# Performance work log

Measured on AMD Instinct MI355X. Metric: run time of the kernel, lower is better.

Reference implementation:

```python
import jax, jax.numpy as jnp
import numpy as np
import math

IMG_SIZE = 768
NUM_CLASSES = 90
THRESHOLD = 0.05
IOU_THRESHOLD = 0.5
MAX_DETECTIONS = 100
K_CAND = 512  # per-class candidate pool before greedy NMS
RATIOS = [(1.0, 1.0), (1.4, 0.7), (0.7, 1.4)]
SCALES = [2 ** 0, 2 ** (1.0 / 3.0), 2 ** (2.0 / 3.0)]


def _generate_anchors():
    anchor_scale = 4.0
    pyramid_levels = [3, 4, 5, 6, 7]
    all_levels = []
    for lv in pyramid_levels:
        stride = 2 ** lv
        size = anchor_scale * 2 ** lv
        grid = IMG_SIZE // stride
        sx = np.arange(grid) * stride
        sy, sx = np.meshgrid(np.arange(grid) * stride, sx, indexing='ij')
        # torch meshgrid(shift_y, shift_x, indexing='ij') -> rows are y
        yy, xx = np.meshgrid(np.arange(grid) * stride, np.arange(grid) * stride, indexing='ij')
        shifts = np.stack([xx.ravel(), yy.ravel(), xx.ravel(), yy.ravel()], axis=1).astype(np.float32)
        base = []
        for r in RATIOS:
            for s in SCALES:
                w = size * s * math.sqrt(r[0] / r[1])
                h = size * s * math.sqrt(r[1] / r[0])
                base.append([-w / 2, -h / 2, w / 2, h / 2])
        base = np.asarray(base, dtype=np.float32)  # [9,4]
        anc = (base[None, :, :] + shifts[:, None, :]).reshape(-1, 4)
        all_levels.append(anc)
    return np.concatenate(all_levels, axis=0)  # [110484,4]


def setup_inputs() -> dict:
    key = jax.random.key(0)
    k1, k2, k3 = jax.random.split(key, 3)
    A = 110484
    x = jax.random.normal(k1, (1, 3, IMG_SIZE, IMG_SIZE), dtype=jnp.float32)
    regression = jax.random.normal(k2, (1, A, 4), dtype=jnp.float32) * 0.3
    classification = jax.random.normal(k3, (1, A, NUM_CLASSES), dtype=jnp.float32) - 2.0
    anchors = jnp.asarray(_generate_anchors())
    return {"x": x, "regression": regression, "classification": classification, "anchors": anchors}


def _decode_and_clip(anchors, deltas, H, W):
    # BBoxTransform (RetinaNet-style): deltas = (dx, dy, dw, dh)
    wa = anchors[:, 2] - anchors[:, 0]
    ha = anchors[:, 3] - anchors[:, 1]
    cxa = anchors[:, 0] + 0.5 * wa
    cya = anchors[:, 1] + 0.5 * ha
    dx, dy, dw, dh = deltas[:, 0], deltas[:, 1], deltas[:, 2], deltas[:, 3]
    cx = cxa + dx * wa
    cy = cya + dy * ha
    w = jnp.exp(dw) * wa
    h = jnp.exp(dh) * ha
    x1 = jnp.clip(cx - 0.5 * w, 0.0, W)
    y1 = jnp.clip(cy - 0.5 * h, 0.0, H)
    x2 = jnp.clip(cx + 0.5 * w, 0.0, W)
    y2 = jnp.clip(cy + 0.5 * h, 0.0, H)
    return jnp.stack([x1, y1, x2, y2], axis=1)  # [A,4]


def _pairwise_iou(b):  # [K,4] -> [K,K]
    area = (b[:, 2] - b[:, 0]) * (b[:, 3] - b[:, 1])
    xx1 = jnp.maximum(b[:, None, 0], b[None, :, 0])
    yy1 = jnp.maximum(b[:, None, 1], b[None, :, 1])
    xx2 = jnp.minimum(b[:, None, 2], b[None, :, 2])
    yy2 = jnp.minimum(b[:, None, 3], b[None, :, 3])
    inter = jnp.clip(xx2 - xx1, 0.0) * jnp.clip(yy2 - yy1, 0.0)
    return inter / (area[:, None] + area[None, :] - inter + 1e-8)


def _greedy_nms(iou_c, valid_c):
    # boxes are pre-sorted by descending score; fixed-iteration greedy NMS
    def step(suppressed, i):
        keep_i = valid_c[i] & jnp.logical_not(suppressed[i])
        suppressed = jnp.where(keep_i, suppressed | (iou_c[i] > IOU_THRESHOLD), suppressed)
        return suppressed, keep_i
    _, keep = jax.lax.scan(step, jnp.zeros(iou_c.shape[0], dtype=bool), jnp.arange(iou_c.shape[0]))
    return keep  # [K]


def _postprocess(x, regression, classification, anchors):
    H, W = x.shape[2], x.shape[3]
    boxes = _decode_and_clip(anchors, regression[0], float(H), float(W))  # [A,4]
    scores = jax.nn.sigmoid(classification[0])                            # [A,C]
    # per-class top-K candidate pool (sorted desc), fixed-shape NMS
    vals, idx = jax.lax.top_k(scores.T, K_CAND)        # [C,K]
    cand = boxes[idx]                                   # [C,K,4]
    valid = vals > THRESHOLD                            # [C,K]
    iou = jax.vmap(_pairwise_iou)(cand)                 # [C,K,K]
    keep = jax.vmap(_greedy_nms)(iou, valid)            # [C,K]
    kept_scores = jnp.where(keep, vals, -1.0).reshape(-1)  # [C*K]
    top_vals, flat_idx = jax.lax.top_k(kept_scores, MAX_DETECTIONS)
    labels = (flat_idx // K_CAND).astype(jnp.float32)
    det_boxes = cand.reshape(-1, 4)[flat_idx]
    ok = top_vals > 0.0
    det = jnp.concatenate([
        jnp.zeros((MAX_DETECTIONS, 1), dtype=jnp.float32),  # batch ids (batch=1 -> 0)
        det_boxes,
        top_vals[:, None],
        labels[:, None],
    ], axis=1)  # [100,7]
    return jnp.where(ok[:, None], det, 0.0)


def reference(x, regression, classification, anchors):
    return _postprocess(x, regression, classification, anchors)
```

## Files before the change

kernel.cpp:

```cpp
#include <hip/hip_runtime.h>
#include <math.h>


#define A_N   110484
#define C_N   90
#define KCAND 512
#define NBINS 8192
#define KSH   19
#define MAXDET 100
#define IMG_F 768.0f
#define THRESH 0.05f
#define VTOT  (A_N / 4)
#define SL_CAP 2048
#define KEEP_CAP 100
#define T_BLKS ((A_N + 63) / 64)
#define PD_BLKS ((A_N + 255) / 256)
#define SEL_T 1024
#define FCAP  512

typedef unsigned int u32;
typedef unsigned long long u64;

__device__ __forceinline__ u32 fkey(float f) {
    u32 u = __float_as_uint(f);
    return (u & 0x80000000u) ? ~u : (u | 0x80000000u);
}
__device__ __forceinline__ float unfkey(u32 k) {
    u32 u = (k & 0x80000000u) ? (k ^ 0x80000000u) : ~k;
    return __uint_as_float(u);
}
__device__ __forceinline__ u64 shflx64(u64 v, int m) {
    u32 lo = (u32)__shfl_xor((int)(u32)v, m, 64);
    u32 hi = (u32)__shfl_xor((int)(v >> 32), m, 64);
    return ((u64)hi << 32) | lo;
}

__global__ __launch_bounds__(256)
void prep_kernel(const float* __restrict__ cls,
                 const float* __restrict__ anchors,
                 const float* __restrict__ reg,
                 u32* __restrict__ keysT,
                 float4* __restrict__ boxes) {
    __shared__ u32 tile[64 * 91];
    if (blockIdx.x >= T_BLKS) {
        int a = (blockIdx.x - T_BLKS) * 256 + threadIdx.x;
        if (a < A_N) {
            float4 an = ((const float4*)anchors)[a];
            float4 dl = ((const float4*)reg)[a];
            float wa = an.z - an.x, ha = an.w - an.y;
            float cx = an.x + 0.5f * wa + dl.x * wa;
            float cy = an.y + 0.5f * ha + dl.y * ha;
            float w = expf(dl.z) * wa;
            float h = expf(dl.w) * ha;
            float4 o;
            o.x = fminf(fmaxf(cx - 0.5f * w, 0.0f), IMG_F);
            o.y = fminf(fmaxf(cy - 0.5f * h, 0.0f), IMG_F);
            o.z = fminf(fmaxf(cx + 0.5f * w, 0.0f), IMG_F);
            o.w = fminf(fmaxf(cy + 0.5f * h, 0.0f), IMG_F);
            boxes[a] = o;
        }
        return;
    }
    const int a0 = blockIdx.x * 64;
    const int lim = min(64, A_N - a0);
    const int n4 = (lim * C_N) >> 2;
    const float4* src4 = (const float4*)(cls + (size_t)a0 * C_N);
    for (int i4 = threadIdx.x; i4 < n4; i4 += 256) {
        float4 x4 = src4[i4];
        const u32 base = (u32)(4 * i4);
        float xs[4] = { x4.x, x4.y, x4.z, x4.w };
        #pragma unroll
        for (int k = 0; k < 4; ++k) {
            u32 i = base + k;
            u32 aa = i / C_N, c = i % C_N;
            float s = 1.0f / (1.0f + expf(-xs[k]));
            tile[aa * 91 + c] = fkey(s);
        }
    }
    __syncthreads();
    for (int j = threadIdx.x; j < C_N * 64; j += 256) {
        int c = j >> 6, aa = j & 63;
        if (aa < lim)
            keysT[(size_t)c * A_N + a0 + aa] = tile[aa * 91 + c];
    }
}

__global__ __launch_bounds__(SEL_T)
void select_kernel(const u32* __restrict__ keysT,
                   u64* __restrict__ candbuf) {
    __shared__ u32 hist[NBINS / 2];
    __shared__ u32 csum[SEL_T];
    __shared__ u64 lbuf[SL_CAP];
    __shared__ u32 sPv;
    __shared__ int lcnt;
    const int tid = threadIdx.x;
    const int c = blockIdx.x;
    const uint4* kv = (const uint4*)(keysT + (size_t)c * A_N);

    for (int i = tid; i < NBINS / 2; i += SEL_T) hist[i] = 0;
    if (tid == 0) { sPv = 0; lcnt = 0; }
    __syncthreads();

    #define HACC(K) do { \
        u32 b0 = (K).x >> KSH, b1 = (K).y >> KSH, b2 = (K).z >> KSH, b3 = (K).w >> KSH; \
        atomicAdd(&hist[b0 >> 1], 1u << ((b0 & 1) << 4)); \
        atomicAdd(&hist[b1 >> 1], 1u << ((b1 & 1) << 4)); \
        atomicAdd(&hist[b2 >> 1], 1u << ((b2 & 1) << 4)); \
        atomicAdd(&hist[b3 >> 1], 1u << ((b3 & 1) << 4)); } while (0)
    {
        int i = tid;
        for (; i + 7 * SEL_T < VTOT; i += 8 * SEL_T) {
            uint4 k0 = kv[i], k1 = kv[i + SEL_T], k2 = kv[i + 2 * SEL_T], k3 = kv[i + 3 * SEL_T];
            uint4 k4 = kv[i + 4 * SEL_T], k5 = kv[i + 5 * SEL_T], k6 = kv[i + 6 * SEL_T], k7 = kv[i + 7 * SEL_T];
            HACC(k0); HACC(k1); HACC(k2); HACC(k3);
            HACC(k4); HACC(k5); HACC(k6); HACC(k7);
        }
        for (; i < VTOT; i += SEL_T) { uint4 ka = kv[i]; HACC(ka); }
    }
    __syncthreads();

    u32 own = 0;
    {
        const int wb = (NBINS / 2) - 4 - 4 * tid;
        const int g = (tid >> 3) & 3;
        #pragma unroll
        for (int jj = 0; jj < 4; ++jj) {
            u32 v = hist[wb + ((g + jj) & 3)];
            own += (v & 0xffffu) + (v >> 16);
        }
    }
    csum[tid] = own;
    __syncthreads();
    for (int off = 1; off < SEL_T; off <<= 1) {
        u32 v = csum[tid];
        u32 a = (tid >= off) ? csum[tid - off] : 0u;
        __syncthreads();
        csum[tid] = v + a;
        __syncthreads();
    }
    const u32 incl = csum[tid], excl = incl - own;
    if (excl < (u32)KCAND && incl >= (u32)KCAND) {
        u32 cum = excl;
        const int hb = NBINS - 1 - 8 * tid;
        for (int j = 0; j < 8; ++j) {
            int b = hb - j;
            u32 v = hist[b >> 1];
            u32 cnt = (b & 1) ? (v >> 16) : (v & 0xffffu);
            if (cum + cnt >= (u32)KCAND) { sPv = (u32)b; break; }
            cum += cnt;
        }
    }
    __syncthreads();
    const u32 P = sPv;

    #define CACC(K, BASE) do { \
        if (((K).x >> KSH) >= P) { int p = atomicAdd(&lcnt, 1); if (p < SL_CAP) lbuf[p] = (((u64)(~(K).x)) << 32) | (u32)(BASE); } \
        if (((K).y >> KSH) >= P) { int p = atomicAdd(&lcnt, 1); if (p < SL_CAP) lbuf[p] = (((u64)(~(K).y)) << 32) | (u32)((BASE) + 1); } \
        if (((K).z >> KSH) >= P) { int p = atomicAdd(&lcnt, 1); if (p < SL_CAP) lbuf[p] = (((u64)(~(K).z)) << 32) | (u32)((BASE) + 2); } \
        if (((K).w >> KSH) >= P) { int p = atomicAdd(&lcnt, 1); if (p < SL_CAP) lbuf[p] = (((u64)(~(K).w)) << 32) | (u32)((BASE) + 3); } } while (0)
    {
        int i = tid;
        for (; i + 7 * SEL_T < VTOT; i += 8 * SEL_T) {
            uint4 k0 = kv[i], k1 = kv[i + SEL_T], k2 = kv[i + 2 * SEL_T], k3 = kv[i + 3 * SEL_T];
            uint4 k4 = kv[i + 4 * SEL_T], k5 = kv[i + 5 * SEL_T], k6 = kv[i + 6 * SEL_T], k7 = kv[i + 7 * SEL_T];
            CACC(k0, 4 * i); CACC(k1, 4 * (i + SEL_T)); CACC(k2, 4 * (i + 2 * SEL_T)); CACC(k3, 4 * (i + 3 * SEL_T));
            CACC(k4, 4 * (i + 4 * SEL_T)); CACC(k5, 4 * (i + 5 * SEL_T)); CACC(k6, 4 * (i + 6 * SEL_T)); CACC(k7, 4 * (i + 7 * SEL_T));
        }
        for (; i < VTOT; i += SEL_T) { uint4 ka = kv[i]; CACC(ka, 4 * i); }
    }
    __syncthreads();
    const int n = min(lcnt, SL_CAP);
    for (int q = tid; q < SL_CAP; q += SEL_T) if (q >= n) lbuf[q] = ~0ULL;
    __syncthreads();

    {
        const int l = tid & 63, w = tid >> 6;
        const int i0 = 128 * w + l, i1 = i0 + 64;
        u64 v0 = lbuf[i0], v1 = lbuf[i1];
        __syncthreads();
        #pragma unroll
        for (u32 kk = 2; kk <= (u32)SL_CAP; kk <<= 1) {
            #pragma unroll
            for (u32 j = kk >> 1; j > 0; j >>= 1) {
                if (j >= 128) {
                    lbuf[i0] = v0; lbuf[i1] = v1;
                    __syncthreads();
                    u64 w0 = lbuf[i0 ^ j], w1 = lbuf[i1 ^ j];
                    bool m0 = (((i0 & j) == 0) == ((i0 & kk) == 0));
                    bool m1 = (((i1 & j) == 0) == ((i1 & kk) == 0));
                    v0 = m0 ? (v0 < w0 ? v0 : w0) : (v0 > w0 ? v0 : w0);
                    v1 = m1 ? (v1 < w1 ? v1 : w1) : (v1 > w1 ? v1 : w1);
                    __syncthreads();
                } else if (j == 64) {
                    bool up = ((i0 & kk) == 0);
                    u64 mn = v0 < v1 ? v0 : v1, mx = v0 < v1 ? v1 : v0;
                    v0 = up ? mn : mx; v1 = up ? mx : mn;
                } else {
                    u64 w0 = shflx64(v0, (int)j), w1 = shflx64(v1, (int)j);
                    bool m0 = (((i0 & j) == 0) == ((i0 & kk) == 0));
                    bool m1 = (((i1 & j) == 0) == ((i1 & kk) == 0));
                    v0 = m0 ? (v0 < w0 ? v0 : w0) : (v0 > w0 ? v0 : w0);
                    v1 = m1 ? (v1 < w1 ? v1 : w1) : (v1 > w1 ? v1 : w1);
                }
            }
        }
        if (w < 4) {
            u64* cb = candbuf + (size_t)c * KCAND;
            cb[i0] = v0; cb[i1] = v1;
        }
    }
}

__global__ __launch_bounds__(1024, 4)
void nms_kernel(const u64* __restrict__ candbuf,
                const float4* __restrict__ boxes,
                u32* __restrict__ keptbuf, u32* __restrict__ cnt2) {
    __shared__ u32 bmask[KCAND * 16];
    __shared__ float4 bb4[KCAND];
    __shared__ float sc[KCAND];
    __shared__ u32 keepf[16], wbase[17];
    const int c = blockIdx.x, tid = threadIdx.x;
    const int l = tid & 63, w = tid >> 6;

    if (tid < KCAND) {
        u64 e = candbuf[(size_t)c * KCAND + tid];
        sc[tid] = unfkey(~((u32)(e >> 32)));
        bb4[tid] = boxes[(u32)e];
    }
    if (tid < 16) keepf[tid] = 0;
    __syncthreads();

    {
        const float4 cj0 = bb4[0 * 64 + l], cj1 = bb4[1 * 64 + l];
        const float4 cj2 = bb4[2 * 64 + l], cj3 = bb4[3 * 64 + l];
        const float4 cj4 = bb4[4 * 64 + l], cj5 = bb4[5 * 64 + l];
        const float4 cj6 = bb4[6 * 64 + l], cj7 = bb4[7 * 64 + l];
        const float aj0 = (cj0.z - cj0.x) * (cj0.w - cj0.y);
        const float aj1 = (cj1.z - cj1.x) * (cj1.w - cj1.y);
        const float aj2 = (cj2.z - cj2.x) * (cj2.w - cj2.y);
        const float aj3 = (cj3.z - cj3.x) * (cj3.w - cj3.y);
        const float aj4 = (cj4.z - cj4.x) * (cj4.w - cj4.y);
        const float aj5 = (cj5.z - cj5.x) * (cj5.w - cj5.y);
        const float aj6 = (cj6.z - cj6.x) * (cj6.w - cj6.y);
        const float aj7 = (cj7.z - cj7.x) * (cj7.w - cj7.y);

        #define QSTEP(QQ, CJ, AJ) do { \
            if (QQ >= q0) { \
                float xx1 = fmaxf(bi.x, (CJ).x), yy1 = fmaxf(bi.y, (CJ).y); \
                float xx2 = fminf(bi.z, (CJ).z), yy2 = fminf(bi.w, (CJ).w); \
                float inter = fmaxf(xx2 - xx1, 0.0f) * fmaxf(yy2 - yy1, 0.0f); \
                float uni = ai + (AJ) - inter + 1e-8f; \
                bool sup = ((QQ * 64 + l) > r) && (inter > 0.5f * uni); \
                u64 bal = __ballot(sup); \
                if (l == 0) *(u64*)(row + 2 * QQ) = bal; \
            } } while (0)

        for (int r = w; r < KCAND; r += 16) {
            const float4 bi = bb4[r];
            const float ai = (bi.z - bi.x) * (bi.w - bi.y);
            const int q0 = (r + 1) >> 6;
            u32* row = bmask + r * 16;
            if (l < 2 * q0) row[l] = 0;
            QSTEP(0, cj0, aj0); QSTEP(1, cj1, aj1);
            QSTEP(2, cj2, aj2); QSTEP(3, cj3, aj3);
            QSTEP(4, cj4, aj4); QSTEP(5, cj5, aj5);
            QSTEP(6, cj6, aj6); QSTEP(7, cj7, aj7);
        }
        #undef QSTEP
    }
    __syncthreads();

    if (tid < 64) {
        const int lw = tid & 15;
        u32 removed = 0, keepw = 0;
        u32 rA[8], rB[8]; float sA[8], sB[8];
        #pragma unroll
        for (int k = 0; k < 8; ++k) { rA[k] = bmask[k * 16 + lw]; sA[k] = sc[k]; }
        #pragma unroll 1
        for (int ch = 0; ch < 64; ch += 2) {
            const int tb1 = (ch + 1) * 8;
            #pragma unroll
            for (int k = 0; k < 8; ++k) { rB[k] = bmask[(tb1 + k) * 16 + lw]; sB[k] = sc[tb1 + k]; }
            {
                const int tb = ch * 8;
                #pragma unroll
                for (int k = 0; k < 8; ++k) {
                    const int t = tb + k;
                    u32 rw = (u32)__builtin_amdgcn_readlane((int)removed, t >> 5);
                    bool d = (sA[k] > THRESH) && (((rw >> (t & 31)) & 1u) == 0u);
                    removed |= d ? rA[k] : 0u;
                    keepw |= (d && (tid == (t >> 5))) ? (1u << (t & 31)) : 0u;
                }
            }
            const int tb2 = (ch + 2 < 64) ? (ch + 2) * 8 : 0;
            #pragma unroll
            for (int k = 0; k < 8; ++k) { rA[k] = bmask[(tb2 + k) * 16 + lw]; sA[k] = sc[tb2 + k]; }
            {
                #pragma unroll
                for (int k = 0; k < 8; ++k) {
                    const int t = tb1 + k;
                    u32 rw = (u32)__builtin_amdgcn_readlane((int)removed, t >> 5);
                    bool d = (sB[k] > THRESH) && (((rw >> (t & 31)) & 1u) == 0u);
                    removed |= d ? rB[k] : 0u;
                    keepw |= (d && (tid == (t >> 5))) ? (1u << (t & 31)) : 0u;
                }
            }
            u32 cnt = (u32)__popc(keepw);
            #pragma unroll
            for (int m = 32; m; m >>= 1) cnt += (u32)__shfl_xor((int)cnt, m, 64);
            if (cnt >= (u32)KEEP_CAP) break;
        }
        if (tid < 16) keepf[tid] = keepw;
    }
    __syncthreads();

    if (tid == 0) {
        u32 t = 0;
        for (int q = 0; q < 16; ++q) { wbase[q] = t; t += __popc(keepf[q]); }
        wbase[16] = t;
        cnt2[c] = (t < (u32)KEEP_CAP) ? t : (u32)KEEP_CAP;
    }
    __syncthreads();
    if (tid < KCAND) {
        u32 word = keepf[tid >> 5];
        u32 bit = (u32)tid & 31u;
        if ((word >> bit) & 1u) {
            u32 rank = wbase[tid >> 5] + __popc(word & ((1u << bit) - 1u));
            if (rank < (u32)KEEP_CAP) {
                float s = sc[tid];
                float4 b = bb4[tid];
                uint4 a2, b2;
                a2.x = ~fkey(s);
                a2.y = (u32)(c * KCAND + tid);
                a2.z = __float_as_uint(b.x);
                a2.w = __float_as_uint(b.y);
                b2.x = __float_as_uint(b.z);
                b2.y = __float_as_uint(b.w);
                b2.z = __float_as_uint(s);
                b2.w = 0u;
                uint4* e = (uint4*)(keptbuf + ((size_t)c * KEEP_CAP + rank) * 8);
                e[0] = a2; e[1] = b2;
            }
        }
    }
}

__global__ __launch_bounds__(1024)
void final_kernel(const u32* __restrict__ keptbuf, const u32* __restrict__ cnt2,
                  float* __restrict__ out) {
    __shared__ u32 hist[NBINS];
    __shared__ u32 csum[1024];
    __shared__ u64 ebuf[FCAP];
    __shared__ u32 eidx[FCAP];
    __shared__ u32 scnt[C_N];
    __shared__ u32 sP;
    __shared__ int sN;
    const int tid = threadIdx.x;
    const int TOT = C_N * KEEP_CAP;

    for (int i = tid; i < MAXDET * 7; i += 1024) out[i] = 0.0f;
    for (int i = tid; i < NBINS; i += 1024) hist[i] = 0;
    if (tid < C_N) scnt[tid] = cnt2[tid];
    if (tid == 0) { sN = 0; sP = NBINS - 1; }
    __syncthreads();

    for (int i = tid; i < TOT; i += 1024) {
        u32 c = (u32)i / KEEP_CAP, pp = (u32)i % KEEP_CAP;
        if (pp < scnt[c]) {
            u32 khi = keptbuf[(size_t)i * 8];
            atomicAdd(&hist[khi >> KSH], 1u);
        }
    }
    __syncthreads();
    u32 own = 0; const int lo = 8 * tid;
    #pragma unroll
    for (int j = 0; j < 8; ++j) own += hist[lo + j];
    csum[tid] = own;
    __syncthreads();
    for (int off = 1; off < 1024; off <<= 1) {
        u32 v = csum[tid];
        u32 a = (tid >= off) ? csum[tid - off] : 0u;
        __syncthreads();
        csum[tid] = v + a;
        __syncthreads();
    }
    const u32 incl = csum[tid], excl = incl - own;
    if (excl < (u32)MAXDET && incl >= (u32)MAXDET) {
        u32 cum = excl;
        for (int j = 0; j < 8; ++j) {
            u32 h = hist[lo + j];
            if (cum + h >= (u32)MAXDET) { sP = (u32)(lo + j); break; }
            cum += h;
        }
    }
    __syncthreads();
    const u32 P = sP;
    for (int i = tid; i < TOT; i += 1024) {
        u32 c = (u32)i / KEEP_CAP, pp = (u32)i % KEEP_CAP;
        if (pp < scnt[c]) {
            const uint2 v2 = *((const uint2*)(keptbuf + (size_t)i * 8));
            if ((v2.x >> KSH) <= P) {
                int p = atomicAdd(&sN, 1);
                if (p < FCAP) {
                    ebuf[p] = ((u64)v2.x << 32) | v2.y;
                    eidx[p] = (u32)i;
                }
            }
        }
    }
    __syncthreads();
    const int n = min(sN, FCAP);
    u32 m = 128; while ((int)m < n) m <<= 1;
    for (int i = tid; i < (int)m; i += 1024) if (i >= n) ebuf[i] = ~0ULL;
    __syncthreads();
    for (u32 kk = 2; kk <= m; kk <<= 1) {
        for (u32 j = kk >> 1; j > 0; j >>= 1) {
            u32 i = (u32)tid;
            if (i < m) {
                u32 ixj = i ^ j;
                if (ixj > i) {
                    u64 x = ebuf[i], y = ebuf[ixj];
                    bool up = ((i & kk) == 0);
                    if (up ? (x > y) : (x < y)) {
                        ebuf[i] = y; ebuf[ixj] = x;
                        u32 t = eidx[i]; eidx[i] = eidx[ixj]; eidx[ixj] = t;
                    }
                }
            }
            __syncthreads();
        }
    }
    if (tid < MAXDET && tid < n) {
        u64 comp = ebuf[tid];
        if (comp != ~0ULL) {
            const uint4* e = (const uint4*)(keptbuf + (size_t)eidx[tid] * 8);
            uint4 a = e[0], b = e[1];
            float* o = out + tid * 7;
            o[0] = 0.0f;
            o[1] = __uint_as_float(a.z); o[2] = __uint_as_float(a.w);
            o[3] = __uint_as_float(b.x); o[4] = __uint_as_float(b.y);
            o[5] = __uint_as_float(b.z);
            o[6] = (float)(((u32)comp) >> 9);
        }
    }
}

extern "C" void kernel_launch(void* const* d_in, const int* in_sizes, int n_in,
                              void* d_out, int out_size, void* d_ws, size_t ws_size,
                              hipStream_t stream) {
    const float* reg     = (const float*)d_in[1];
    const float* cls     = (const float*)d_in[2];
    const float* anchors = (const float*)d_in[3];
    float* out = (float*)d_out;

    char* ws = (char*)d_ws;
    size_t off = 0;
    auto alloc = [&](size_t bytes) -> void* {
        void* p = ws + off;
        off = (off + bytes + 255) & ~(size_t)255;
        return p;
    };
    u32*    keysT   = (u32*)   alloc((size_t)C_N * A_N * sizeof(u32));
    float4* boxes   = (float4*)alloc((size_t)A_N * sizeof(float4));
    u64*    candbuf = (u64*)   alloc((size_t)C_N * KCAND * sizeof(u64));
    u32*    keptbuf = (u32*)   alloc((size_t)C_N * KEEP_CAP * 8 * sizeof(u32));
    u32*    cnt2    = (u32*)   alloc((size_t)C_N * sizeof(u32));
    (void)ws_size;

    prep_kernel<<<T_BLKS + PD_BLKS, 256, 0, stream>>>(cls, anchors, reg, keysT, boxes);
    select_kernel<<<C_N, SEL_T, 0, stream>>>(keysT, candbuf);
    nms_kernel<<<C_N, 1024, 0, stream>>>(candbuf, boxes, keptbuf, cnt2);
    final_kernel<<<1, 1024, 0, stream>>>(keptbuf, cnt2, out);
}
```

Measured before the change: 190.1 us.

## Fuse per-class top-K selection and NMS into one kernel with aliased shared memory

Merges the select and NMS kernels into a single per-class block. The sorted candidates stay in registers and are scattered straight into shared score and box arrays, so the candbuf global round trip and one kernel launch go away. Shared memory is one aliased buffer reused between the histogram/sort phase and the NMS bitmask phase. The NMS phase inherits the select kernel's launch bounds and register pressure, and the aliasing relies on correct barriers between phases.

```diff
diff --git a/kernel.cpp b/kernel.cpp
--- a/kernel.cpp
+++ b/kernel.cpp
@@ -85,16 +85,24 @@
     }
 }
 
-__global__ __launch_bounds__(SEL_T)
-void select_kernel(const u32* __restrict__ keysT,
-                   u64* __restrict__ candbuf) {
-    __shared__ u32 hist[NBINS / 2];
-    __shared__ u32 csum[SEL_T];
-    __shared__ u64 lbuf[SL_CAP];
+__global__ __launch_bounds__(SEL_T, 4)
+void selnms_kernel(const u32* __restrict__ keysT,
+                   const float4* __restrict__ boxes,
+                   u32* __restrict__ keptbuf, u32* __restrict__ cnt2) {
+    __shared__ __align__(16) u32 smem[11264];
+    u32* hist = smem;
+    u32* csum = smem + 4096;
+    u64* lbuf = (u64*)(smem + 5120);
+    float4* bb4 = (float4*)smem;
+    float* sc = (float*)(smem + 2048);
+    u32* keepf = smem + 2560;
+    u32* wbase = smem + 2576;
+    u32* bmask = smem + 2608;
     __shared__ u32 sPv;
     __shared__ int lcnt;
     const int tid = threadIdx.x;
     const int c = blockIdx.x;
+    const int l = tid & 63, w = tid >> 6;
     const uint4* kv = (const uint4*)(keysT + (size_t)c * A_N);
 
     for (int i = tid; i < NBINS / 2; i += SEL_T) hist[i] = 0;
@@ -173,10 +181,10 @@
     for (int q = tid; q < SL_CAP; q += SEL_T) if (q >= n) lbuf[q] = ~0ULL;
     __syncthreads();
 
+    const int i0 = 128 * w + l, i1 = i0 + 64;
+    u64 v0, v1;
     {
-        const int l = tid & 63, w = tid >> 6;
-        const int i0 = 128 * w + l, i1 = i0 + 64;
-        u64 v0 = lbuf[i0], v1 = lbuf[i1];
+        v0 = lbuf[i0]; v1 = lbuf[i1];
         __syncthreads();
         #pragma unroll
         for (u32 kk = 2; kk <= (u32)SL_CAP; kk <<= 1) {
@@ -204,28 +212,14 @@
                 }
             }
         }
-        if (w < 4) {
-            u64* cb = candbuf + (size_t)c * KCAND;
-            cb[i0] = v0; cb[i1] = v1;
-        }
-    }
-}
-
-__global__ __launch_bounds__(1024, 4)
-void nms_kernel(const u64* __restrict__ candbuf,
-                const float4* __restrict__ boxes,
-                u32* __restrict__ keptbuf, u32* __restrict__ cnt2) {
-    __shared__ u32 bmask[KCAND * 16];
-    __shared__ float4 bb4[KCAND];
-    __shared__ float sc[KCAND];
-    __shared__ u32 keepf[16], wbase[17];
-    const int c = blockIdx.x, tid = threadIdx.x;
-    const int l = tid & 63, w = tid >> 6;
-
-    if (tid < KCAND) {
-        u64 e = candbuf[(size_t)c * KCAND + tid];
-        sc[tid] = unfkey(~((u32)(e >> 32)));
-        bb4[tid] = boxes[(u32)e];
+    }
+    __syncthreads();
+
+    if (w < 4) {
+        sc[i0] = unfkey(~((u32)(v0 >> 32)));
+        sc[i1] = unfkey(~((u32)(v1 >> 32)));
+        bb4[i0] = boxes[(u32)v0];
+        bb4[i1] = boxes[(u32)v1];
     }
     if (tid < 16) keepf[tid] = 0;
     __syncthreads();
@@ -462,13 +456,11 @@
     };
     u32*    keysT   = (u32*)   alloc((size_t)C_N * A_N * sizeof(u32));
     float4* boxes   = (float4*)alloc((size_t)A_N * sizeof(float4));
-    u64*    candbuf = (u64*)   alloc((size_t)C_N * KCAND * sizeof(u64));
     u32*    keptbuf = (u32*)   alloc((size_t)C_N * KEEP_CAP * 8 * sizeof(u32));
     u32*    cnt2    = (u32*)   alloc((size_t)C_N * sizeof(u32));
     (void)ws_size;
 
     prep_kernel<<<T_BLKS + PD_BLKS, 256, 0, stream>>>(cls, anchors, reg, keysT, boxes);
-    select_kernel<<<C_N, SEL_T, 0, stream>>>(keysT, candbuf);
-    nms_kernel<<<C_N, 1024, 0, stream>>>(candbuf, boxes, keptbuf, cnt2);
+    selnms_kernel<<<C_N, SEL_T, 0, stream>>>(keysT, boxes, keptbuf, cnt2);
     final_kernel<<<1, 1024, 0, stream>>>(keptbuf, cnt2, out);
 }
```

After: 188.2 us. No clear change (-1.0%).
